# Performance work log

Measured on AMD Instinct MI355X. Metric: run time of the kernel, lower is better.

Reference implementation:

```python
import jax, jax.numpy as jnp
import numpy as np

N = 33554432  # number of elements
POS_WEIGHT = 1.0
NEG_WEIGHT = 8.0
EPS = 1e-07


def setup_inputs() -> dict:
    key = jax.random.key(0)
    k1, k2 = jax.random.split(key)
    outputs = jax.random.uniform(k1, (N,), dtype=jnp.float32)  # probabilities in (0,1)
    targets = jax.random.randint(k2, (N,), 0, 2, dtype=jnp.int32)  # binary labels
    return {"outputs": outputs, "targets": targets}


def reference(outputs, targets):
    # weight-select, log, and mean-reduction in one fused elementwise pass
    pos = POS_WEIGHT * -jnp.log(outputs + EPS)
    neg = NEG_WEIGHT * -jnp.log(1.0 - outputs + EPS)
    loss = jnp.where(targets == 1, pos, neg)
    return jnp.mean(loss)
```

## Files before the change

kernel.cpp:

```cpp
#include <hip/hip_runtime.h>

#define NEG_W 8.0f
#define EPS 1e-7f
#define BLOCKS 2048
#define TPB 256

__global__ __launch_bounds__(TPB) void bce_partial(
    const float4* __restrict__ out4, const int4* __restrict__ tgt4,
    double* __restrict__ partials, int nvec) {
  float sum = 0.0f;
  const int stride = gridDim.x * blockDim.x;
  for (int i = blockIdx.x * blockDim.x + threadIdx.x; i < nvec; i += stride) {
    float4 o = out4[i];
    int4 t = tgt4[i];
    float x0 = (t.x == 1) ? (o.x + EPS) : (1.0f - o.x + EPS);
    float w0 = (t.x == 1) ? 1.0f : NEG_W;
    float x1 = (t.y == 1) ? (o.y + EPS) : (1.0f - o.y + EPS);
    float w1 = (t.y == 1) ? 1.0f : NEG_W;
    float x2 = (t.z == 1) ? (o.z + EPS) : (1.0f - o.z + EPS);
    float w2 = (t.z == 1) ? 1.0f : NEG_W;
    float x3 = (t.w == 1) ? (o.w + EPS) : (1.0f - o.w + EPS);
    float w3 = (t.w == 1) ? 1.0f : NEG_W;
    sum = fmaf(w0, __logf(x0), sum);
    sum = fmaf(w1, __logf(x1), sum);
    sum = fmaf(w2, __logf(x2), sum);
    sum = fmaf(w3, __logf(x3), sum);
  }
  sum = -sum;

  for (int off = 32; off > 0; off >>= 1)
    sum += __shfl_down(sum, off, 64);

  __shared__ float wsum[TPB / 64];
  const int lane = threadIdx.x & 63;
  const int wid = threadIdx.x >> 6;
  if (lane == 0) wsum[wid] = sum;
  __syncthreads();
  if (threadIdx.x == 0) {
    float s = 0.0f;
    for (int w = 0; w < TPB / 64; ++w) s += wsum[w];
    partials[blockIdx.x] = (double)s;
  }
}

__global__ __launch_bounds__(TPB) void bce_finalize(
    const double* __restrict__ partials, float* __restrict__ out, int nblocks,
    float inv_n) {
  double s = 0.0;
  for (int i = threadIdx.x; i < nblocks; i += TPB) s += partials[i];
  for (int off = 32; off > 0; off >>= 1)
    s += __shfl_down(s, off, 64);
  __shared__ double wsum[TPB / 64];
  const int lane = threadIdx.x & 63;
  const int wid = threadIdx.x >> 6;
  if (lane == 0) wsum[wid] = s;
  __syncthreads();
  if (threadIdx.x == 0) {
    double tot = 0.0;
    for (int w = 0; w < TPB / 64; ++w) tot += wsum[w];
    out[0] = (float)(tot * (double)inv_n);
  }
}

extern "C" void kernel_launch(void* const* d_in, const int* in_sizes, int n_in,
                              void* d_out, int out_size, void* d_ws, size_t ws_size,
                              hipStream_t stream) {
  const float4* out4 = (const float4*)d_in[0];
  const int4* tgt4 = (const int4*)d_in[1];
  const int n = in_sizes[0];
  const int nvec = n / 4;
  double* partials = (double*)d_ws;

  bce_partial<<<BLOCKS, TPB, 0, stream>>>(out4, tgt4, partials, nvec);
  bce_finalize<<<1, TPB, 0, stream>>>(partials, (float*)d_out, BLOCKS,
                                      1.0f / (float)n);
}
```

Before: 277.5 us.

## Replace grid-stride loop with one-shot blocks issuing all loads up front

The partial kernel drops the grid-stride loop and instead launches 8192 blocks, each handling a fixed 1024-vector chunk. Every thread issues four float4 and four int4 loads before any compute, then uses four independent accumulators. The goal is more memory-level parallelism for this bandwidth-bound reduction. The kernel now assumes the element count is exactly BLOCKS*TPB*VPT*4 with no bounds check, which holds only for this input size. Partials are stored as float and summed in double in the finalize kernel.

```diff
diff --git a/kernel.cpp b/kernel.cpp
--- a/kernel.cpp
+++ b/kernel.cpp
@@ -2,31 +2,41 @@
 
 #define NEG_W 8.0f
 #define EPS 1e-7f
-#define BLOCKS 2048
 #define TPB 256
+#define VPT 4
+#define BLOCKS 8192
 
 __global__ __launch_bounds__(TPB) void bce_partial(
     const float4* __restrict__ out4, const int4* __restrict__ tgt4,
-    double* __restrict__ partials, int nvec) {
-  float sum = 0.0f;
-  const int stride = gridDim.x * blockDim.x;
-  for (int i = blockIdx.x * blockDim.x + threadIdx.x; i < nvec; i += stride) {
-    float4 o = out4[i];
-    int4 t = tgt4[i];
-    float x0 = (t.x == 1) ? (o.x + EPS) : (1.0f - o.x + EPS);
-    float w0 = (t.x == 1) ? 1.0f : NEG_W;
-    float x1 = (t.y == 1) ? (o.y + EPS) : (1.0f - o.y + EPS);
-    float w1 = (t.y == 1) ? 1.0f : NEG_W;
-    float x2 = (t.z == 1) ? (o.z + EPS) : (1.0f - o.z + EPS);
-    float w2 = (t.z == 1) ? 1.0f : NEG_W;
-    float x3 = (t.w == 1) ? (o.w + EPS) : (1.0f - o.w + EPS);
-    float w3 = (t.w == 1) ? 1.0f : NEG_W;
-    sum = fmaf(w0, __logf(x0), sum);
-    sum = fmaf(w1, __logf(x1), sum);
-    sum = fmaf(w2, __logf(x2), sum);
-    sum = fmaf(w3, __logf(x3), sum);
+    float* __restrict__ partials, int nvec) {
+  const int base = blockIdx.x * (TPB * VPT) + threadIdx.x;
+
+  float4 o[VPT];
+  int4 t[VPT];
+#pragma unroll
+  for (int u = 0; u < VPT; ++u) {
+    const int idx = base + u * TPB;
+    o[u] = out4[idx];
+    t[u] = tgt4[idx];
   }
-  sum = -sum;
+
+  float acc0 = 0.0f, acc1 = 0.0f, acc2 = 0.0f, acc3 = 0.0f;
+#pragma unroll
+  for (int u = 0; u < VPT; ++u) {
+    float x0 = (t[u].x == 1) ? (o[u].x + EPS) : (1.0f - o[u].x + EPS);
+    float w0 = (t[u].x == 1) ? 1.0f : NEG_W;
+    float x1 = (t[u].y == 1) ? (o[u].y + EPS) : (1.0f - o[u].y + EPS);
+    float w1 = (t[u].y == 1) ? 1.0f : NEG_W;
+    float x2 = (t[u].z == 1) ? (o[u].z + EPS) : (1.0f - o[u].z + EPS);
+    float w2 = (t[u].z == 1) ? 1.0f : NEG_W;
+    float x3 = (t[u].w == 1) ? (o[u].w + EPS) : (1.0f - o[u].w + EPS);
+    float w3 = (t[u].w == 1) ? 1.0f : NEG_W;
+    acc0 = fmaf(w0, __logf(x0), acc0);
+    acc1 = fmaf(w1, __logf(x1), acc1);
+    acc2 = fmaf(w2, __logf(x2), acc2);
+    acc3 = fmaf(w3, __logf(x3), acc3);
+  }
+  float sum = -((acc0 + acc1) + (acc2 + acc3));
 
   for (int off = 32; off > 0; off >>= 1)
     sum += __shfl_down(sum, off, 64);
@@ -39,15 +49,15 @@
   if (threadIdx.x == 0) {
     float s = 0.0f;
     for (int w = 0; w < TPB / 64; ++w) s += wsum[w];
-    partials[blockIdx.x] = (double)s;
+    partials[blockIdx.x] = s;
   }
 }
 
 __global__ __launch_bounds__(TPB) void bce_finalize(
-    const double* __restrict__ partials, float* __restrict__ out, int nblocks,
-    float inv_n) {
+    const float* __restrict__ partials, float* __restrict__ out, int nblocks,
+    double inv_n) {
   double s = 0.0;
-  for (int i = threadIdx.x; i < nblocks; i += TPB) s += partials[i];
+  for (int i = threadIdx.x; i < nblocks; i += TPB) s += (double)partials[i];
   for (int off = 32; off > 0; off >>= 1)
     s += __shfl_down(s, off, 64);
   __shared__ double wsum[TPB / 64];
@@ -58,7 +68,7 @@
   if (threadIdx.x == 0) {
     double tot = 0.0;
     for (int w = 0; w < TPB / 64; ++w) tot += wsum[w];
-    out[0] = (float)(tot * (double)inv_n);
+    out[0] = (float)(tot * inv_n);
   }
 }
 
@@ -69,9 +79,9 @@
   const int4* tgt4 = (const int4*)d_in[1];
   const int n = in_sizes[0];
   const int nvec = n / 4;
-  double* partials = (double*)d_ws;
+  float* partials = (float*)d_ws;
 
   bce_partial<<<BLOCKS, TPB, 0, stream>>>(out4, tgt4, partials, nvec);
   bce_finalize<<<1, TPB, 0, stream>>>(partials, (float*)d_out, BLOCKS,
-                                      1.0f / (float)n);
+                                      1.0 / (double)n);
 }
```

Measured after the change: 277.6 us. No clear change (+0.1%).
